# Kernel tuning notes

Measured on AMD Instinct MI355X. Metric: run time of the kernel, lower is better.

Reference implementation:

```python
import jax, jax.numpy as jnp
import numpy as np

NUM_RELATIONS = 3


def _rgcn(x, W_rel, W_root, bias, src, dst, etype):
    # PyG RGCNConv: out = x @ W_root + bias + sum_r mean_{e: type(e)=r, dst(e)=i} (x_src @ W_r)
    n = x.shape[0]
    xr = jnp.einsum('ni,rio->rno', x, W_rel)          # [R, N, F] relation-transformed nodes
    msg = xr[etype, src]                               # [E, F] per-edge messages
    out = x @ W_root + bias
    for r in range(NUM_RELATIONS):
        m = (etype == r)
        s = jax.ops.segment_sum(jnp.where(m[:, None], msg, 0.0), dst, num_segments=n)
        c = jax.ops.segment_sum(m.astype(x.dtype), dst, num_segments=n)
        out = out + s / jnp.maximum(c, 1.0)[:, None]   # mean aggregation per relation
    return out


def _gate(h, q, Wg, bg, Wq, bq):
    # h: [BN, F], q: [B, L, F]
    B, L, F = q.shape
    N = h.shape[0] // B
    h3 = h.reshape(B, N, F)
    # w_gate(cat([h_i, q_l])) = h_i @ Wg[:, :F].T + q_l @ Wg[:, F:].T + bg
    hg = jnp.einsum('bnf,gf->bng', h3, Wg[:, :F])                    # [B,N,F]
    qg = jnp.einsum('blf,gf->blg', q, Wg[:, F:]) + bg                # [B,L,F]
    attn = jax.nn.sigmoid(hg[:, :, None, :] + qg[:, None, :, :])     # [B,N,L,F]
    qi = jnp.einsum('bnlf,blf->bnf', attn, q)                        # [B,N,F]
    alpha = jax.nn.sigmoid(
        jnp.einsum('bnf,gf->bng', h3, Wq[:, :F])
        + jnp.einsum('bnf,gf->bng', qi, Wq[:, F:]) + bq)
    hn = alpha * jnp.tanh(qi) + (1.0 - alpha) * h3
    return hn.reshape(B * N, F)


def setup_inputs() -> dict:
    key = jax.random.key(0)
    ks = jax.random.split(key, 16)
    F = 768
    BN, E, B, L = 2048, 65536, 8, 64
    s = 0.02
    return {
        'x': jax.random.normal(ks[0], (BN, F), jnp.float32),
        'edge_index': jax.random.randint(ks[1], (2, E), 0, BN),
        'edge_type': jax.random.randint(ks[2], (E,), 0, NUM_RELATIONS),
        'query_embs': jax.random.normal(ks[3], (B, L, F), jnp.float32),
        'W_rel1': jax.random.normal(ks[4], (NUM_RELATIONS, F, F), jnp.float32) * s,
        'W_root1': jax.random.normal(ks[5], (F, F), jnp.float32) * s,
        'b1': jnp.zeros((F,), jnp.float32),
        'W_rel2': jax.random.normal(ks[6], (NUM_RELATIONS, F, F), jnp.float32) * s,
        'W_root2': jax.random.normal(ks[7], (F, F), jnp.float32) * s,
        'b2': jnp.zeros((F,), jnp.float32),
        'Wg': jax.random.normal(ks[8], (F, 2 * F), jnp.float32) * s,
        'bg': jnp.zeros((F,), jnp.float32),
        'Wq': jax.random.normal(ks[9], (F, 2 * F), jnp.float32) * s,
        'bq': jnp.zeros((F,), jnp.float32),
    }


def reference(x, edge_index, edge_type, query_embs,
              W_rel1, W_root1, b1, W_rel2, W_root2, b2, Wg, bg, Wq, bq):
    src, dst = edge_index[0], edge_index[1]
    h = jax.nn.relu(_rgcn(x, W_rel1, W_root1, b1, src, dst, edge_type))
    h = _gate(h, query_embs, Wg, bg, Wq, bq)
    h = jax.nn.relu(_rgcn(h, W_rel2, W_root2, b2, src, dst, edge_type))
    h = _gate(h, query_embs, Wg, bg, Wq, bq)
    return h
```

## Files before the change

kernel.cpp:

```cpp
#include <hip/hip_runtime.h>
#include <hip/hip_bf16.h>
#include <cstdint>
#include <cstddef>

#define F 768

typedef float f32x4 __attribute__((ext_vector_type(4)));
typedef short s16x8 __attribute__((ext_vector_type(8)));
typedef short s16x4 __attribute__((ext_vector_type(4)));

#define NEG_LOG2E (-1.4426950408889634f)

__device__ __forceinline__ float bf2f(unsigned short u) {
  union { unsigned int i; float f; } v; v.i = ((unsigned int)u) << 16; return v.f;
}
__device__ __forceinline__ unsigned short f2bf(float f) {
  union { float f; unsigned int i; } v; v.f = f;
  unsigned int r = v.i + 0x7FFF + ((v.i >> 16) & 1);
  return (unsigned short)(r >> 16);
}

#if __has_builtin(__builtin_amdgcn_exp2f)
__device__ __forceinline__ float fexp2(float x) { return __builtin_amdgcn_exp2f(x); }
#else
__device__ __forceinline__ float fexp2(float x) { return exp2f(x); }
#endif
#if __has_builtin(__builtin_amdgcn_rcpf)
__device__ __forceinline__ float frcp(float x) { return __builtin_amdgcn_rcpf(x); }
#else
__device__ __forceinline__ float frcp(float x) { return 1.0f / x; }
#endif

__device__ __forceinline__ float ftanh(float x) {
  float t = fexp2(x * 2.8853900817779268f);
  float s = frcp(t + 1.0f);
  return fmaf(-2.0f, s, 1.0f);
}

__device__ __forceinline__ void gload16(const void* g, void* l) {
  __builtin_amdgcn_global_load_lds(
      (const __attribute__((address_space(1))) void*)g,
      (__attribute__((address_space(3))) void*)l, 16, 0, 0);
}

__global__ void khist(const int* __restrict__ ei, int E, int* __restrict__ cnt) {
  int e = blockIdx.x * blockDim.x + threadIdx.x;
  if (e < E) atomicAdd(&cnt[ei[E + e]], 1);
}

__global__ void kscan(const int* __restrict__ cnt, int* __restrict__ offs, int n) {
  __shared__ int part[256];
  int t = threadIdx.x;
  const int per = n / 256;
  int local[8];
  int s = 0;
  for (int j = 0; j < per; ++j) { local[j] = cnt[t * per + j]; s += local[j]; }
  part[t] = s;
  __syncthreads();
  for (int d = 1; d < 256; d <<= 1) {
    int v = (t >= d) ? part[t - d] : 0;
    __syncthreads();
    part[t] += v;
    __syncthreads();
  }
  int run = (t == 0) ? 0 : part[t - 1];
  for (int j = 0; j < per; ++j) { offs[t * per + j] = run; run += local[j]; }
  if (t == 255) offs[n] = run;
}

__global__ void kscatter(const int* __restrict__ ei, const int* __restrict__ et, int E,
                         const int* __restrict__ offs, int* __restrict__ cur,
                         int* __restrict__ sorted) {
  int e = blockIdx.x * blockDim.x + threadIdx.x;
  if (e >= E) return;
  int dst = ei[E + e];
  int pos = offs[dst] + atomicAdd(&cur[dst], 1);
  sorted[pos] = ei[e] | (et[e] << 16);
}

__global__ void kcvt(const float* __restrict__ x, const float* __restrict__ q, int nx,
                     unsigned short* __restrict__ Acat, unsigned short* __restrict__ qbf) {
  const int r = blockIdx.x, c = threadIdx.x * 4;
  const float* srow;
  unsigned short* drow;
  if (r < nx) { srow = x + (size_t)r * F; drow = Acat + (size_t)r * 3072; }
  else        { srow = q + (size_t)(r - nx) * F; drow = qbf + (size_t)(r - nx) * F; }
  float4 v = *(const float4*)(srow + c);
  s16x4 o;
  o[0] = (short)f2bf(v.x); o[1] = (short)f2bf(v.y);
  o[2] = (short)f2bf(v.z); o[3] = (short)f2bf(v.w);
  *(s16x4*)(drow + c) = o;
}

__global__ void kcvtw(const float* __restrict__ Wg, const float* __restrict__ Wq,
                      unsigned short* __restrict__ Wgq, unsigned short* __restrict__ WgR,
                      unsigned short* __restrict__ WqR) {
  const int b = blockIdx.x, c = threadIdx.x * 4;
  const float* srow;
  unsigned short* drow;
  int off;
  if (b < 1536) {
    srow = (b < 768) ? Wg + (size_t)b * 1536 : Wq + (size_t)(b - 768) * 1536;
    drow = Wgq + (size_t)b * 768;
    off = 0;
  } else if (b < 2304) {
    srow = Wg + (size_t)(b - 1536) * 1536;
    drow = WgR + (size_t)(b - 1536) * 768;
    off = 768;
  } else {
    srow = Wq + (size_t)(b - 2304) * 1536;
    drow = WqR + (size_t)(b - 2304) * 768;
    off = 768;
  }
  float4 v = *(const float4*)(srow + off + c);
  s16x4 o;
  o[0] = (short)f2bf(v.x); o[1] = (short)f2bf(v.y);
  o[2] = (short)f2bf(v.z); o[3] = (short)f2bf(v.w);
  *(s16x4*)(drow + c) = o;
}

__global__ void ktrans(const float* __restrict__ Wr1, const float* __restrict__ Wl1,
                       const float* __restrict__ Wr2, const float* __restrict__ Wl2,
                       unsigned short* __restrict__ Wcat1, unsigned short* __restrict__ Wcat2) {
  __shared__ float tile[64][65];
  const int z = blockIdx.z, layer = z >> 2, part = z & 3;
  const float* src = (part == 0) ? (layer ? Wr2 : Wr1)
                                 : ((layer ? Wl2 : Wl1) + (size_t)(part - 1) * F * F);
  unsigned short* dst = (layer ? Wcat2 : Wcat1) + part * F;
  const int kt = blockIdx.x * 64, nt = blockIdx.y * 64;
  const int t = threadIdx.x, c = t & 63, r4 = t >> 6;
#pragma unroll
  for (int it = 0; it < 16; ++it) {
    int kk = r4 + it * 4;
    tile[kk][c] = src[(size_t)(kt + kk) * F + nt + c];
  }
  __syncthreads();
#pragma unroll
  for (int it = 0; it < 16; ++it) {
    int rr = r4 + it * 4;
    dst[(size_t)(nt + rr) * 3072 + kt + c] = f2bf(tile[c][rr]);
  }
}

__global__ void kagg(const int* __restrict__ offs, const int* __restrict__ sorted,
                     const unsigned short* __restrict__ hin,
                     unsigned short* __restrict__ dst) {
  const int i = blockIdx.x, t = threadIdx.x;
  const int col = t * 4;
  float a0[4] = {}, a1[4] = {}, a2[4] = {};
  int c0 = 0, c1 = 0, c2 = 0;
  const int beg = offs[i], end = offs[i + 1];
  int e = beg;
  for (; e + 3 < end; e += 4) {
    int pk[4];
#pragma unroll
    for (int u = 0; u < 4; ++u) pk[u] = sorted[e + u];
    s16x4 w[4];
#pragma unroll
    for (int u = 0; u < 4; ++u)
      w[u] = *(const s16x4*)(hin + (size_t)(pk[u] & 0xFFFF) * 3072 + col);
#pragma unroll
    for (int u = 0; u < 4; ++u) {
      int r = pk[u] >> 16;
      float v[4];
#pragma unroll
      for (int j = 0; j < 4; ++j) v[j] = bf2f((unsigned short)w[u][j]);
      if (r == 0)      { c0++; for (int j = 0; j < 4; ++j) a0[j] += v[j]; }
      else if (r == 1) { c1++; for (int j = 0; j < 4; ++j) a1[j] += v[j]; }
      else             { c2++; for (int j = 0; j < 4; ++j) a2[j] += v[j]; }
    }
  }
  for (; e < end; ++e) {
    int p0 = sorted[e];
    s16x4 w0 = *(const s16x4*)(hin + (size_t)(p0 & 0xFFFF) * 3072 + col);
    int r0 = p0 >> 16;
    float v0[4];
#pragma unroll
    for (int j = 0; j < 4; ++j) v0[j] = bf2f((unsigned short)w0[j]);
    if (r0 == 0)      { c0++; for (int j = 0; j < 4; ++j) a0[j] += v0[j]; }
    else if (r0 == 1) { c1++; for (int j = 0; j < 4; ++j) a1[j] += v0[j]; }
    else              { c2++; for (int j = 0; j < 4; ++j) a2[j] += v0[j]; }
  }
  const float i0 = frcp((float)(c0 > 0 ? c0 : 1));
  const float i1 = frcp((float)(c1 > 0 ? c1 : 1));
  const float i2 = frcp((float)(c2 > 0 ? c2 : 1));
  unsigned short* d = dst + (size_t)i * 3072 + col;
  s16x4 o;
#pragma unroll
  for (int j = 0; j < 4; ++j) o[j] = (short)f2bf(a0[j] * i0);
  *(s16x4*)d = o;
#pragma unroll
  for (int j = 0; j < 4; ++j) o[j] = (short)f2bf(a1[j] * i1);
  *(s16x4*)(d + F) = o;
#pragma unroll
  for (int j = 0; j < 4; ++j) o[j] = (short)f2bf(a2[j] * i2);
  *(s16x4*)(d + 2 * F) = o;
}

template <int EPI>
__launch_bounds__(512)
__global__ void kmm(const unsigned short* __restrict__ A, int lda,
                    const unsigned short* __restrict__ B, int ldb,
                    float* __restrict__ C, int ldc, int K,
                    const float* __restrict__ bias,
                    const float* __restrict__ aux1,
                    const unsigned short* __restrict__ aux2,
                    unsigned short* __restrict__ C2, int ldc2,
                    float escale, int Lq) {
  __shared__ unsigned short Asb[2][64 * 64];
  __shared__ unsigned short Bsb[2][64 * 64];
  const int t = threadIdx.x;
  const int lane = t & 63, wid = t >> 6;
  const int wr = wid >> 2, wc = wid & 3;
  const int bm = blockIdx.x * 64, bn = blockIdx.y * 64;

  const int srow = t >> 3, schunk = t & 7;
  const int kxor = ((schunk ^ (srow & 7)) << 3);
  const unsigned short* Ap = A + (size_t)(bm + srow) * lda + kxor;
  const unsigned short* Bp = B + (size_t)(bn + srow) * ldb + kxor;

  const int rA0 = wr * 32 + (lane & 15);
  const int rB0 = wc * 16 + (lane & 15);
  const int l7 = lane & 7, lq = lane >> 4;
  const int s8_0 = (((0 * 4 + lq) ^ l7) << 3);
  const int s8_1 = (((1 * 4 + lq) ^ l7) << 3);

  f32x4 acc[2] = {};

  auto stage = [&](int cb, int k0) {
    gload16(Ap + k0, &Asb[cb][t * 8]);
    gload16(Bp + k0, &Bsb[cb][t * 8]);
  };

  stage(0, 0);
  __syncthreads();
  int cur = 0;
  for (int k0 = 0; k0 < K; k0 += 64) {
    if (k0 + 64 < K) stage(cur ^ 1, k0 + 64);
    const unsigned short* As = Asb[cur];
    const unsigned short* Bs = Bsb[cur];
#pragma unroll
    for (int ks = 0; ks < 2; ++ks) {
      const int s8 = ks ? s8_1 : s8_0;
      s16x8 af[2], bf;
#pragma unroll
      for (int i = 0; i < 2; ++i)
        af[i] = *(const s16x8*)(As + (rA0 + i * 16) * 64 + s8);
      bf = *(const s16x8*)(Bs + rB0 * 64 + s8);
#pragma unroll
      for (int i = 0; i < 2; ++i)
        acc[i] = __builtin_amdgcn_mfma_f32_16x16x32_bf16(af[i], bf, acc[i], 0, 0, 0);
    }
    __syncthreads();
    cur ^= 1;
  }

  const int colw = bn + wc * 16 + (lane & 15);

  if (EPI == 7 && bn < 768) {
    float hgp[2][4], qacc[2][4];
#pragma unroll
    for (int i = 0; i < 2; ++i)
#pragma unroll
      for (int j = 0; j < 4; ++j) {
        hgp[i][j] = acc[i][j] * NEG_LOG2E;
        qacc[i][j] = 0.0f;
      }
    const int b = bm >> 8;
    const float* qb = aux1 + (size_t)b * Lq * F;
    const float* qgb = bias + (size_t)b * Lq * F;
#pragma unroll 4
    for (int l = 0; l < Lq; ++l) {
      const float qg0 = qgb[(size_t)l * F + colw];
      const float q0 = qb[(size_t)l * F + colw];
#pragma unroll
      for (int i = 0; i < 2; ++i)
#pragma unroll
        for (int j = 0; j < 4; ++j)
          qacc[i][j] = fmaf(frcp(1.0f + fexp2(hgp[i][j] + qg0)), q0, qacc[i][j]);
    }
#pragma unroll
    for (int i = 0; i < 2; ++i)
#pragma unroll
      for (int j = 0; j < 4; ++j) {
        const int row = bm + wr * 32 + i * 16 + (lane >> 4) * 4 + j;
        C2[(size_t)row * 768 + colw] = f2bf(qacc[i][j]);
        C[(size_t)row * 1536 + colw] = ftanh(qacc[i][j]);
      }
    return;
  }

#pragma unroll
  for (int i = 0; i < 2; ++i)
#pragma unroll
    for (int j = 0; j < 4; ++j) {
      const int row = bm + wr * 32 + i * 16 + (lane >> 4) * 4 + j;
      const int col = colw;
      float v = acc[i][j];
      if (EPI == 3 || EPI == 4) {
        float zh = aux1[(size_t)row * 1536 + 768 + col];
        float z = v + bias[col] + zh;
        float al = frcp(1.0f + fexp2(z * NEG_LOG2E));
        float tq = aux1[(size_t)row * 1536 + col];
        float hv = bf2f(aux2[(size_t)row * 768 + col]);
        float o = al * tq + (1.0f - al) * hv;
        if (EPI == 3) C2[(size_t)row * ldc2 + col] = f2bf(o);
        else          C[(size_t)row * ldc + col] = o;
      } else if (EPI == 6) {
        C[(size_t)row * ldc + col] = (v + bias[col]) * escale;
      } else {
        C[(size_t)row * ldc + col] = v;
      }
    }
}

__launch_bounds__(512)
__global__ void kmm_pk(const unsigned short* __restrict__ A, int lda,
                       const unsigned short* __restrict__ B, int ldb,
                       float* __restrict__ P, int Ksplit, int pstride) {
  __shared__ unsigned short Asb[2][64 * 64];
  __shared__ unsigned short Bsb[2][64 * 64];
  const int t = threadIdx.x;
  const int lane = t & 63, wid = t >> 6;
  const int wr = wid >> 2, wc = wid & 3;
  const int bm = blockIdx.x * 64, bn = blockIdx.y * 64;
  const int kbase = blockIdx.z * Ksplit;
  float* Cp = P + (size_t)blockIdx.z * pstride;

  const int srow = t >> 3, schunk = t & 7;
  const int kxor = ((schunk ^ (srow & 7)) << 3);
  const unsigned short* Ap = A + (size_t)(bm + srow) * lda + kxor + kbase;
  const unsigned short* Bp = B + (size_t)(bn + srow) * ldb + kxor + kbase;

  const int rA0 = wr * 32 + (lane & 15);
  const int rB0 = wc * 16 + (lane & 15);
  const int l7 = lane & 7, lq = lane >> 4;
  const int s8_0 = (((0 * 4 + lq) ^ l7) << 3);
  const int s8_1 = (((1 * 4 + lq) ^ l7) << 3);

  f32x4 acc[2] = {};

  auto stage = [&](int cb, int k0) {
    gload16(Ap + k0, &Asb[cb][t * 8]);
    gload16(Bp + k0, &Bsb[cb][t * 8]);
  };

  stage(0, 0);
  __syncthreads();
  int cur = 0;
  for (int k0 = 0; k0 < Ksplit; k0 += 64) {
    if (k0 + 64 < Ksplit) stage(cur ^ 1, k0 + 64);
    const unsigned short* As = Asb[cur];
    const unsigned short* Bs = Bsb[cur];
#pragma unroll
    for (int ks = 0; ks < 2; ++ks) {
      const int s8 = ks ? s8_1 : s8_0;
      s16x8 af[2], bf;
#pragma unroll
      for (int i = 0; i < 2; ++i)
        af[i] = *(const s16x8*)(As + (rA0 + i * 16) * 64 + s8);
      bf = *(const s16x8*)(Bs + rB0 * 64 + s8);
#pragma unroll
      for (int i = 0; i < 2; ++i)
        acc[i] = __builtin_amdgcn_mfma_f32_16x16x32_bf16(af[i], bf, acc[i], 0, 0, 0);
    }
    __syncthreads();
    cur ^= 1;
  }

  const int col = bn + wc * 16 + (lane & 15);
#pragma unroll
  for (int i = 0; i < 2; ++i)
#pragma unroll
    for (int j = 0; j < 4; ++j) {
      const int row = bm + wr * 32 + i * 16 + (lane >> 4) * 4 + j;
      Cp[(size_t)row * F + col] = acc[i][j];
    }
}

__global__ void kep_relu(const float* __restrict__ P, int pstride,
                         const float* __restrict__ bias,
                         unsigned short* __restrict__ hb) {
  const int idx = (blockIdx.x * 256 + threadIdx.x) * 4;
  const int col = idx - (idx / F) * F;
  float4 s = *(const float4*)(P + idx);
  const float4 s1 = *(const float4*)(P + pstride + idx);
  const float4 s2 = *(const float4*)(P + 2 * (size_t)pstride + idx);
  const float4 s3 = *(const float4*)(P + 3 * (size_t)pstride + idx);
  const float4 bv = *(const float4*)(bias + col);
  s.x = fmaxf(s.x + s1.x + s2.x + s3.x + bv.x, 0.0f);
  s.y = fmaxf(s.y + s1.y + s2.y + s3.y + bv.y, 0.0f);
  s.z = fmaxf(s.z + s1.z + s2.z + s3.z + bv.z, 0.0f);
  s.w = fmaxf(s.w + s1.w + s2.w + s3.w + bv.w, 0.0f);
  s16x4 o;
  o[0] = (short)f2bf(s.x); o[1] = (short)f2bf(s.y);
  o[2] = (short)f2bf(s.z); o[3] = (short)f2bf(s.w);
  *(s16x4*)(hb + idx) = o;
}

extern "C" void kernel_launch(void* const* d_in, const int* in_sizes, int n_in,
                              void* d_out, int out_size, void* d_ws, size_t ws_size,
                              hipStream_t stream) {
  const float* x = (const float*)d_in[0];
  const int* ei = (const int*)d_in[1];
  const int* et = (const int*)d_in[2];
  const float* q = (const float*)d_in[3];
  const float* Wrel1 = (const float*)d_in[4];
  const float* Wroot1 = (const float*)d_in[5];
  const float* b1 = (const float*)d_in[6];
  const float* Wrel2 = (const float*)d_in[7];
  const float* Wroot2 = (const float*)d_in[8];
  const float* b2 = (const float*)d_in[9];
  const float* Wg = (const float*)d_in[10];
  const float* bg = (const float*)d_in[11];
  const float* Wq = (const float*)d_in[12];
  const float* bq = (const float*)d_in[13];

  const int BNn = in_sizes[0] / F;
  const int E = in_sizes[1] / 2;
  const int L = 64;
  const int Bq = in_sizes[3] / (L * F);
  const int ML = Bq * L;
  const int PSTR = BNn * F;
  float* out = (float*)d_out;

  char* p = (char*)d_ws;
  auto alloc = [&](size_t bytes) {
    void* r = (void*)p;
    p += (bytes + 255) & ~(size_t)255;
    return r;
  };
  int* cntcur = (int*)alloc((size_t)2 * BNn * 4);
  int* cnt = cntcur;
  int* cur = cntcur + BNn;
  int* offs = (int*)alloc((size_t)(BNn + 1) * 4);
  int* sorted = (int*)alloc((size_t)E * 4);
  unsigned short* Acat = (unsigned short*)alloc((size_t)BNn * 3072 * 2);
  unsigned short* Wcat1 = (unsigned short*)alloc((size_t)F * 3072 * 2);
  unsigned short* Wcat2 = (unsigned short*)alloc((size_t)F * 3072 * 2);
  unsigned short* Wgq = (unsigned short*)alloc((size_t)1536 * F * 2);
  unsigned short* WgR = (unsigned short*)alloc((size_t)F * F * 2);
  unsigned short* WqR = (unsigned short*)alloc((size_t)F * F * 2);
  unsigned short* qbf = (unsigned short*)alloc((size_t)ML * F * 2);
  float* qg = (float*)alloc((size_t)ML * F * 4);
  unsigned short* hb = (unsigned short*)alloc((size_t)BNn * F * 2);
  float* hgz = (float*)alloc((size_t)BNn * 1536 * 4);
  unsigned short* qib = (unsigned short*)alloc((size_t)BNn * F * 2);
  float* parts = (float*)alloc((size_t)4 * PSTR * 4);

  hipMemsetAsync(cntcur, 0, (size_t)2 * BNn * 4, stream);
  khist<<<(E + 255) / 256, 256, 0, stream>>>(ei, E, cnt);
  kscan<<<1, 256, 0, stream>>>(cnt, offs, BNn);
  kscatter<<<(E + 255) / 256, 256, 0, stream>>>(ei, et, E, offs, cur, sorted);

  kcvt<<<BNn + ML, 192, 0, stream>>>(x, q, BNn, Acat, qbf);
  kcvtw<<<3072, 192, 0, stream>>>(Wg, Wq, Wgq, WgR, WqR);
  ktrans<<<dim3(12, 12, 8), 256, 0, stream>>>(Wroot1, Wrel1, Wroot2, Wrel2, Wcat1, Wcat2);

  kmm<6><<<dim3(ML / 64, F / 64), 512, 0, stream>>>(
      qbf, F, WgR, F, qg, F, F, bg, nullptr, nullptr, nullptr, 0, NEG_LOG2E, L);

  for (int layer = 0; layer < 2; ++layer) {
    const unsigned short* Wcat = layer ? Wcat2 : Wcat1;
    const float* bb = layer ? b2 : b1;

    kagg<<<BNn, 192, 0, stream>>>(offs, sorted, Acat, Acat + F);

    kmm_pk<<<dim3(BNn / 64, F / 64, 4), 512, 0, stream>>>(
        Acat, 3072, Wcat, 3072, parts, F, PSTR);

    kep_relu<<<(BNn * F) / 1024, 256, 0, stream>>>(parts, PSTR, bb, hb);

    kmm<7><<<dim3(BNn / 64, 1536 / 64), 512, 0, stream>>>(
        hb, F, Wgq, F, hgz, 1536, F, qg, q, nullptr, qib, F, 0.f, L);

    if (layer == 0) {
      kmm<3><<<dim3(BNn / 64, F / 64), 512, 0, stream>>>(
          qib, F, WqR, F, nullptr, 0, F, bq, hgz, hb, Acat, 3072, 0.f, L);
    } else {
      kmm<4><<<dim3(BNn / 64, F / 64), 512, 0, stream>>>(
          qib, F, WqR, F, out, F, F, bq, hgz, hb, nullptr, 0, 0.f, L);
    }
  }
}
```

Baseline: 318.0 us.

## Factor gate exponentials, halve split-K partials, merge conversion kernels, store tanh as bf16

The gate attention now precomputes exp(-hg) and exp(-qg) once, so each inner-loop term is one FMA plus a reciprocal instead of an add, exp2 and reciprocal. The clamp keeps the exponent product finite. The RGCN GEMM split-K drops from 4 to 2 partitions, which cuts partial-sum traffic in the ReLU epilogue but gives fewer blocks and longer K loops. The input and weight conversion kernels are merged into a single launch. The tanh(qi) intermediate is stored as bf16 in its own buffer, and the z_h buffer is narrowed to 768 columns, reducing epilogue memory traffic.

```diff
diff --git a/kernel.cpp b/kernel.cpp
--- a/kernel.cpp
+++ b/kernel.cpp
@@ -35,6 +35,9 @@
   float t = fexp2(x * 2.8853900817779268f);
   float s = frcp(t + 1.0f);
   return fmaf(-2.0f, s, 1.0f);
+}
+__device__ __forceinline__ float fclamp60(float x) {
+  return fminf(fmaxf(x, -60.0f), 60.0f);
 }
 
 __device__ __forceinline__ void gload16(const void* g, void* l) {
@@ -78,41 +81,33 @@
   sorted[pos] = ei[e] | (et[e] << 16);
 }
 
-__global__ void kcvt(const float* __restrict__ x, const float* __restrict__ q, int nx,
-                     unsigned short* __restrict__ Acat, unsigned short* __restrict__ qbf) {
-  const int r = blockIdx.x, c = threadIdx.x * 4;
-  const float* srow;
-  unsigned short* drow;
-  if (r < nx) { srow = x + (size_t)r * F; drow = Acat + (size_t)r * 3072; }
-  else        { srow = q + (size_t)(r - nx) * F; drow = qbf + (size_t)(r - nx) * F; }
-  float4 v = *(const float4*)(srow + c);
-  s16x4 o;
-  o[0] = (short)f2bf(v.x); o[1] = (short)f2bf(v.y);
-  o[2] = (short)f2bf(v.z); o[3] = (short)f2bf(v.w);
-  *(s16x4*)(drow + c) = o;
-}
-
-__global__ void kcvtw(const float* __restrict__ Wg, const float* __restrict__ Wq,
+__global__ void kprep(const float* __restrict__ x, const float* __restrict__ q,
+                      const float* __restrict__ Wg, const float* __restrict__ Wq,
+                      int nx, int nq,
+                      unsigned short* __restrict__ Acat, unsigned short* __restrict__ qbf,
                       unsigned short* __restrict__ Wgq, unsigned short* __restrict__ WgR,
                       unsigned short* __restrict__ WqR) {
   const int b = blockIdx.x, c = threadIdx.x * 4;
   const float* srow;
   unsigned short* drow;
-  int off;
-  if (b < 1536) {
-    srow = (b < 768) ? Wg + (size_t)b * 1536 : Wq + (size_t)(b - 768) * 1536;
-    drow = Wgq + (size_t)b * 768;
-    off = 0;
-  } else if (b < 2304) {
-    srow = Wg + (size_t)(b - 1536) * 1536;
-    drow = WgR + (size_t)(b - 1536) * 768;
-    off = 768;
+  if (b < nx) {
+    srow = x + (size_t)b * F; drow = Acat + (size_t)b * 3072;
+  } else if (b < nx + nq) {
+    srow = q + (size_t)(b - nx) * F; drow = qbf + (size_t)(b - nx) * F;
   } else {
-    srow = Wq + (size_t)(b - 2304) * 1536;
-    drow = WqR + (size_t)(b - 2304) * 768;
-    off = 768;
-  }
-  float4 v = *(const float4*)(srow + off + c);
+    const int w = b - nx - nq;
+    if (w < 1536) {
+      srow = (w < 768) ? Wg + (size_t)w * 1536 : Wq + (size_t)(w - 768) * 1536;
+      drow = Wgq + (size_t)w * 768;
+    } else if (w < 2304) {
+      srow = Wg + (size_t)(w - 1536) * 1536 + 768;
+      drow = WgR + (size_t)(w - 1536) * 768;
+    } else {
+      srow = Wq + (size_t)(w - 2304) * 1536 + 768;
+      drow = WqR + (size_t)(w - 2304) * 768;
+    }
+  }
+  float4 v = *(const float4*)(srow + c);
   s16x4 o;
   o[0] = (short)f2bf(v.x); o[1] = (short)f2bf(v.y);
   o[2] = (short)f2bf(v.z); o[3] = (short)f2bf(v.w);
@@ -203,10 +198,11 @@
                     const unsigned short* __restrict__ B, int ldb,
                     float* __restrict__ C, int ldc, int K,
                     const float* __restrict__ bias,
-                    const float* __restrict__ aux1,
-                    const unsigned short* __restrict__ aux2,
+                    const float* __restrict__ auxf,
+                    const unsigned short* __restrict__ hbb,
                     unsigned short* __restrict__ C2, int ldc2,
-                    float escale, int Lq) {
+                    unsigned short* __restrict__ tqb,
+                    int Lq) {
   __shared__ unsigned short Asb[2][64 * 64];
   __shared__ unsigned short Bsb[2][64 * 64];
   const int t = threadIdx.x;
@@ -257,36 +253,46 @@
 
   const int colw = bn + wc * 16 + (lane & 15);
 
-  if (EPI == 7 && bn < 768) {
-    float hgp[2][4], qacc[2][4];
-#pragma unroll
-    for (int i = 0; i < 2; ++i)
-#pragma unroll
-      for (int j = 0; j < 4; ++j) {
-        hgp[i][j] = acc[i][j] * NEG_LOG2E;
-        qacc[i][j] = 0.0f;
+  if (EPI == 7) {
+    if (bn < 768) {
+      float ea[2][4], qacc[2][4];
+#pragma unroll
+      for (int i = 0; i < 2; ++i)
+#pragma unroll
+        for (int j = 0; j < 4; ++j) {
+          ea[i][j] = fexp2(fclamp60(acc[i][j] * NEG_LOG2E));
+          qacc[i][j] = 0.0f;
+        }
+      const int b = bm >> 8;
+      const float* qb = auxf + (size_t)b * Lq * F;
+      const float* qeb = bias + (size_t)b * Lq * F;
+#pragma unroll 4
+      for (int l = 0; l < Lq; ++l) {
+        const float qe = qeb[(size_t)l * F + colw];
+        const float q0 = qb[(size_t)l * F + colw];
+#pragma unroll
+        for (int i = 0; i < 2; ++i)
+#pragma unroll
+          for (int j = 0; j < 4; ++j)
+            qacc[i][j] = fmaf(frcp(fmaf(ea[i][j], qe, 1.0f)), q0, qacc[i][j]);
       }
-    const int b = bm >> 8;
-    const float* qb = aux1 + (size_t)b * Lq * F;
-    const float* qgb = bias + (size_t)b * Lq * F;
-#pragma unroll 4
-    for (int l = 0; l < Lq; ++l) {
-      const float qg0 = qgb[(size_t)l * F + colw];
-      const float q0 = qb[(size_t)l * F + colw];
-#pragma unroll
-      for (int i = 0; i < 2; ++i)
-#pragma unroll
-        for (int j = 0; j < 4; ++j)
-          qacc[i][j] = fmaf(frcp(1.0f + fexp2(hgp[i][j] + qg0)), q0, qacc[i][j]);
-    }
-#pragma unroll
-    for (int i = 0; i < 2; ++i)
-#pragma unroll
-      for (int j = 0; j < 4; ++j) {
-        const int row = bm + wr * 32 + i * 16 + (lane >> 4) * 4 + j;
-        C2[(size_t)row * 768 + colw] = f2bf(qacc[i][j]);
-        C[(size_t)row * 1536 + colw] = ftanh(qacc[i][j]);
-      }
+#pragma unroll
+      for (int i = 0; i < 2; ++i)
+#pragma unroll
+        for (int j = 0; j < 4; ++j) {
+          const int row = bm + wr * 32 + i * 16 + (lane >> 4) * 4 + j;
+          C2[(size_t)row * 768 + colw] = f2bf(qacc[i][j]);
+          tqb[(size_t)row * 768 + colw] = f2bf(ftanh(qacc[i][j]));
+        }
+    } else {
+#pragma unroll
+      for (int i = 0; i < 2; ++i)
+#pragma unroll
+        for (int j = 0; j < 4; ++j) {
+          const int row = bm + wr * 32 + i * 16 + (lane >> 4) * 4 + j;
+          C[(size_t)row * 768 + (colw - 768)] = acc[i][j];
+        }
+    }
     return;
   }
 
@@ -298,18 +304,16 @@
       const int col = colw;
       float v = acc[i][j];
       if (EPI == 3 || EPI == 4) {
-        float zh = aux1[(size_t)row * 1536 + 768 + col];
+        float zh = auxf[(size_t)row * 768 + col];
         float z = v + bias[col] + zh;
         float al = frcp(1.0f + fexp2(z * NEG_LOG2E));
-        float tq = aux1[(size_t)row * 1536 + col];
-        float hv = bf2f(aux2[(size_t)row * 768 + col]);
+        float tq = bf2f(tqb[(size_t)row * 768 + col]);
+        float hv = bf2f(hbb[(size_t)row * 768 + col]);
         float o = al * tq + (1.0f - al) * hv;
         if (EPI == 3) C2[(size_t)row * ldc2 + col] = f2bf(o);
         else          C[(size_t)row * ldc + col] = o;
       } else if (EPI == 6) {
-        C[(size_t)row * ldc + col] = (v + bias[col]) * escale;
-      } else {
-        C[(size_t)row * ldc + col] = v;
+        C[(size_t)row * ldc + col] = fexp2(fclamp60((v + bias[col]) * NEG_LOG2E));
       }
     }
 }
@@ -385,13 +389,11 @@
   const int col = idx - (idx / F) * F;
   float4 s = *(const float4*)(P + idx);
   const float4 s1 = *(const float4*)(P + pstride + idx);
-  const float4 s2 = *(const float4*)(P + 2 * (size_t)pstride + idx);
-  const float4 s3 = *(const float4*)(P + 3 * (size_t)pstride + idx);
   const float4 bv = *(const float4*)(bias + col);
-  s.x = fmaxf(s.x + s1.x + s2.x + s3.x + bv.x, 0.0f);
-  s.y = fmaxf(s.y + s1.y + s2.y + s3.y + bv.y, 0.0f);
-  s.z = fmaxf(s.z + s1.z + s2.z + s3.z + bv.z, 0.0f);
-  s.w = fmaxf(s.w + s1.w + s2.w + s3.w + bv.w, 0.0f);
+  s.x = fmaxf(s.x + s1.x + bv.x, 0.0f);
+  s.y = fmaxf(s.y + s1.y + bv.y, 0.0f);
+  s.z = fmaxf(s.z + s1.z + bv.z, 0.0f);
+  s.w = fmaxf(s.w + s1.w + bv.w, 0.0f);
   s16x4 o;
   o[0] = (short)f2bf(s.x); o[1] = (short)f2bf(s.y);
   o[2] = (short)f2bf(s.z); o[3] = (short)f2bf(s.w);
@@ -442,23 +444,24 @@
   unsigned short* WgR = (unsigned short*)alloc((size_t)F * F * 2);
   unsigned short* WqR = (unsigned short*)alloc((size_t)F * F * 2);
   unsigned short* qbf = (unsigned short*)alloc((size_t)ML * F * 2);
-  float* qg = (float*)alloc((size_t)ML * F * 4);
+  float* qgE = (float*)alloc((size_t)ML * F * 4);
   unsigned short* hb = (unsigned short*)alloc((size_t)BNn * F * 2);
-  float* hgz = (float*)alloc((size_t)BNn * 1536 * 4);
+  float* zhb = (float*)alloc((size_t)BNn * F * 4);
+  unsigned short* tqb = (unsigned short*)alloc((size_t)BNn * F * 2);
   unsigned short* qib = (unsigned short*)alloc((size_t)BNn * F * 2);
-  float* parts = (float*)alloc((size_t)4 * PSTR * 4);
+  float* parts = (float*)alloc((size_t)2 * PSTR * 4);
 
   hipMemsetAsync(cntcur, 0, (size_t)2 * BNn * 4, stream);
   khist<<<(E + 255) / 256, 256, 0, stream>>>(ei, E, cnt);
   kscan<<<1, 256, 0, stream>>>(cnt, offs, BNn);
   kscatter<<<(E + 255) / 256, 256, 0, stream>>>(ei, et, E, offs, cur, sorted);
 
-  kcvt<<<BNn + ML, 192, 0, stream>>>(x, q, BNn, Acat, qbf);
-  kcvtw<<<3072, 192, 0, stream>>>(Wg, Wq, Wgq, WgR, WqR);
+  kprep<<<BNn + ML + 3072, 192, 0, stream>>>(x, q, Wg, Wq, BNn, ML,
+                                             Acat, qbf, Wgq, WgR, WqR);
   ktrans<<<dim3(12, 12, 8), 256, 0, stream>>>(Wroot1, Wrel1, Wroot2, Wrel2, Wcat1, Wcat2);
 
   kmm<6><<<dim3(ML / 64, F / 64), 512, 0, stream>>>(
-      qbf, F, WgR, F, qg, F, F, bg, nullptr, nullptr, nullptr, 0, NEG_LOG2E, L);
+      qbf, F, WgR, F, qgE, F, F, bg, nullptr, nullptr, nullptr, 0, nullptr, L);
 
   for (int layer = 0; layer < 2; ++layer) {
     const unsigned short* Wcat = layer ? Wcat2 : Wcat1;
@@ -466,20 +469,20 @@
 
     kagg<<<BNn, 192, 0, stream>>>(offs, sorted, Acat, Acat + F);
 
-    kmm_pk<<<dim3(BNn / 64, F / 64, 4), 512, 0, stream>>>(
-        Acat, 3072, Wcat, 3072, parts, F, PSTR);
+    kmm_pk<<<dim3(BNn / 64, F / 64, 2), 512, 0, stream>>>(
+        Acat, 3072, Wcat, 3072, parts, 1536, PSTR);
 
     kep_relu<<<(BNn * F) / 1024, 256, 0, stream>>>(parts, PSTR, bb, hb);
 
     kmm<7><<<dim3(BNn / 64, 1536 / 64), 512, 0, stream>>>(
-        hb, F, Wgq, F, hgz, 1536, F, qg, q, nullptr, qib, F, 0.f, L);
+        hb, F, Wgq, F, zhb, F, F, qgE, q, nullptr, qib, F, tqb, L);
 
     if (layer == 0) {
       kmm<3><<<dim3(BNn / 64, F / 64), 512, 0, stream>>>(
-          qib, F, WqR, F, nullptr, 0, F, bq, hgz, hb, Acat, 3072, 0.f, L);
+          qib, F, WqR, F, nullptr, 0, F, bq, zhb, hb, Acat, 3072, tqb, L);
     } else {
       kmm<4><<<dim3(BNn / 64, F / 64), 512, 0, stream>>>(
-          qib, F, WqR, F, out, F, F, bq, hgz, hb, nullptr, 0, 0.f, L);
-    }
-  }
-}
+          qib, F, WqR, F, out, F, F, bq, zhb, hb, nullptr, 0, tqb, L);
+    }
+  }
+}
```

Result: faster. 291.2 us (-8.4%).
